# Kernel optimization log

Measured on AMD Instinct MI355X. Metric: run time of the kernel, lower is better.

## Reference

```python
import jax, jax.numpy as jnp
import numpy as np

H = 1024      # hidden_size
V = 50257     # output_size (vocab)
L = 512       # max_length


def setup_inputs() -> dict:
    key = jax.random.key(0)
    ks = jax.random.split(key, 12)
    s = 0.02
    return {
        "x": jax.random.randint(ks[0], (1,), 0, V),
        "encoder_outputs": jax.random.normal(ks[1], (L, H), jnp.float32),
        "hidden": jax.random.normal(ks[2], (1, 1, H), jnp.float32),
        # parameters
        "emb": jax.random.normal(ks[3], (V, H), jnp.float32) * s,
        "attn_W": jax.random.normal(ks[4], (L, 2 * H), jnp.float32) * s,
        "attn_b": jnp.zeros((L,), jnp.float32),
        "comb_W": jax.random.normal(ks[5], (H, 2 * H), jnp.float32) * s,
        "comb_b": jnp.zeros((H,), jnp.float32),
        "W_ih": jax.random.normal(ks[6], (3 * H, H), jnp.float32) * s,
        "W_hh": jax.random.normal(ks[7], (3 * H, H), jnp.float32) * s,
        "b_ih": jnp.zeros((3 * H,), jnp.float32),
        "b_hh": jnp.zeros((3 * H,), jnp.float32),
        "out_W": jax.random.normal(ks[8], (V, H), jnp.float32) * s,
        "out_b": jnp.zeros((V,), jnp.float32),
    }


def reference(x, encoder_outputs, hidden, emb, attn_W, attn_b, comb_W, comb_b,
              W_ih, W_hh, b_ih, b_hh, out_W, out_b):
    # embedded: [1, H]  (dropout_p=0 -> identity)
    embedded = emb[x]
    h0 = hidden[0]  # [1, H]
    # Bahdanau-style attention over encoder positions
    attn_weights = jax.nn.softmax(
        jnp.concatenate([embedded, h0], axis=1) @ attn_W.T + attn_b, axis=1)  # [1, L]
    attn_applied = attn_weights @ encoder_outputs  # [1, H]
    # combine + relu
    out = jnp.concatenate([embedded, attn_applied], axis=1) @ comb_W.T + comb_b
    out = jax.nn.relu(out)  # [1, H] -- GRU input
    # GRU cell (PyTorch gate ordering: r, z, n)
    gx = out @ W_ih.T + b_ih   # [1, 3H]
    gh = h0 @ W_hh.T + b_hh    # [1, 3H]
    gx_r, gx_z, gx_n = jnp.split(gx, 3, axis=1)
    gh_r, gh_z, gh_n = jnp.split(gh, 3, axis=1)
    r = jax.nn.sigmoid(gx_r + gh_r)
    z = jax.nn.sigmoid(gx_z + gh_z)
    n = jnp.tanh(gx_n + r * gh_n)
    h_new = (1.0 - z) * n + z * h0  # [1, H]
    # output projection + log_softmax
    logp = jax.nn.log_softmax(h_new @ out_W.T + out_b, axis=1)  # [1, V]
    return logp, attn_weights
```

## Files before the change

kernel.cpp:

```cpp
#include <hip/hip_runtime.h>
#include <math.h>

#define H 1024
#define V 50257
#define L 512
#define RPB 32
#define NPART ((V + RPB - 1) / RPB)

__device__ inline float wave_reduce_sum(float v) {
    #pragma unroll
    for (int off = 32; off > 0; off >>= 1)
        v += __shfl_down(v, off, 64);
    return v;
}

__device__ inline float wave_reduce_max(float v) {
    #pragma unroll
    for (int off = 32; off > 0; off >>= 1)
        v = fmaxf(v, __shfl_down(v, off, 64));
    return v;
}

__device__ inline float dot4(float4 a, float4 b) {
    return a.x * b.x + a.y * b.y + a.z * b.z + a.w * b.w;
}

__device__ inline float sigmoidf_(float x) { return 1.f / (1.f + expf(-x)); }

__global__ void k1_scores_gh(const int* __restrict__ x,
                             const float* __restrict__ emb,
                             const float* __restrict__ hidden,
                             const float* __restrict__ attn_W,
                             const float* __restrict__ attn_b,
                             const float* __restrict__ W_hh,
                             const float* __restrict__ b_hh,
                             float* __restrict__ scores,
                             float* __restrict__ gh,
                             float* __restrict__ attnap) {
    const int b = blockIdx.x;
    const int t = threadIdx.x;
    const int lid = t & 63, wid = t >> 6;
    const float4* hv = (const float4*)hidden;
    if (b < 128) {
        const int l = b * 4 + wid;
        const int xi = x[0];
        const float4* ev = (const float4*)(emb + (size_t)xi * H);
        const float4* wrow = (const float4*)(attn_W + (size_t)l * (2 * H));
        float acc = 0.f;
        #pragma unroll
        for (int k = 0; k < 4; ++k) {
            int idx = k * 64 + lid;
            acc += dot4(ev[idx], wrow[idx]);
        }
        #pragma unroll
        for (int k = 0; k < 4; ++k) {
            int idx = k * 64 + lid;
            acc += dot4(hv[idx], wrow[256 + idx]);
        }
        acc = wave_reduce_sum(acc);
        if (lid == 0) scores[l] = acc + attn_b[l];
    } else if (b < 896) {
        const int r = (b - 128) * 4 + wid;
        const float4* wrow = (const float4*)(W_hh + (size_t)r * H);
        float acc = 0.f;
        #pragma unroll
        for (int k = 0; k < 4; ++k) {
            int idx = k * 64 + lid;
            acc += dot4(hv[idx], wrow[idx]);
        }
        acc = wave_reduce_sum(acc);
        if (lid == 0) gh[r] = acc + b_hh[r];
    } else {
        ((float4*)attnap)[t] = make_float4(0.f, 0.f, 0.f, 0.f);
    }
}

__global__ void k2_softmax_apply(const float* __restrict__ scores,
                                 const float* __restrict__ enc,
                                 float* __restrict__ attnap,
                                 float* __restrict__ out_attn) {
    const int t = threadIdx.x;
    __shared__ float smx[4], sms[4], sw[512];
    float v0 = scores[t], v1 = scores[t + 256];
    float m = wave_reduce_max(fmaxf(v0, v1));
    if ((t & 63) == 0) smx[t >> 6] = m;
    __syncthreads();
    float M = fmaxf(fmaxf(smx[0], smx[1]), fmaxf(smx[2], smx[3]));
    float e0 = expf(v0 - M), e1 = expf(v1 - M);
    float s = wave_reduce_sum(e0 + e1);
    if ((t & 63) == 0) sms[t >> 6] = s;
    __syncthreads();
    float S = sms[0] + sms[1] + sms[2] + sms[3];
    float w0 = e0 / S, w1 = e1 / S;
    sw[t] = w0;
    sw[t + 256] = w1;
    if (blockIdx.x == 0 && blockIdx.y == 0) {
        out_attn[t] = w0;
        out_attn[t + 256] = w1;
    }
    __syncthreads();
    const int h = blockIdx.x * 256 + t;
    const int l0 = blockIdx.y * 32;
    float acc = 0.f;
    #pragma unroll 8
    for (int i = 0; i < 32; ++i)
        acc += sw[l0 + i] * enc[(size_t)(l0 + i) * H + h];
    atomicAdd(&attnap[h], acc);
}

__global__ void k3_combine(const int* __restrict__ x,
                           const float* __restrict__ emb,
                           const float* __restrict__ attnap,
                           const float* __restrict__ comb_W,
                           const float* __restrict__ comb_b,
                           float* __restrict__ gru_in) {
    const int t = threadIdx.x;
    const int lid = t & 63, wid = t >> 6;
    const int r = blockIdx.x * 4 + wid;
    const int xi = x[0];
    const float4* ev = (const float4*)(emb + (size_t)xi * H);
    const float4* av = (const float4*)attnap;
    const float4* wrow = (const float4*)(comb_W + (size_t)r * (2 * H));
    float acc = 0.f;
    #pragma unroll
    for (int k = 0; k < 4; ++k) {
        int idx = k * 64 + lid;
        acc += dot4(ev[idx], wrow[idx]);
    }
    #pragma unroll
    for (int k = 0; k < 4; ++k) {
        int idx = k * 64 + lid;
        acc += dot4(av[idx], wrow[256 + idx]);
    }
    acc = wave_reduce_sum(acc);
    if (lid == 0) gru_in[r] = fmaxf(acc + comb_b[r], 0.f);
}

__global__ void k4_gx(const float* __restrict__ W_ih,
                      const float* __restrict__ b_ih,
                      const float* __restrict__ gru_in,
                      float* __restrict__ gx) {
    const int t = threadIdx.x;
    const int lid = t & 63, wid = t >> 6;
    const int r = blockIdx.x * 4 + wid;
    const float4* vv = (const float4*)gru_in;
    const float4* wrow = (const float4*)(W_ih + (size_t)r * H);
    float acc = 0.f;
    #pragma unroll
    for (int k = 0; k < 4; ++k) {
        int idx = k * 64 + lid;
        acc += dot4(vv[idx], wrow[idx]);
    }
    acc = wave_reduce_sum(acc);
    if (lid == 0) gx[r] = acc + b_ih[r];
}

__global__ void k5_cell_logits(const float* __restrict__ gx,
                               const float* __restrict__ gh,
                               const float* __restrict__ hidden,
                               const float* __restrict__ out_W,
                               const float* __restrict__ out_b,
                               float* __restrict__ logits,
                               float* __restrict__ partials) {
    const int t = threadIdx.x;
    __shared__ float sh[H];
    __shared__ float sl[RPB];
    {
        float4 xr = ((const float4*)gx)[t];
        float4 xz = ((const float4*)(gx + H))[t];
        float4 xn = ((const float4*)(gx + 2 * H))[t];
        float4 hr = ((const float4*)gh)[t];
        float4 hz = ((const float4*)(gh + H))[t];
        float4 hn = ((const float4*)(gh + 2 * H))[t];
        float4 h0 = ((const float4*)hidden)[t];
        float4 o;
        {
            float r = sigmoidf_(xr.x + hr.x), z = sigmoidf_(xz.x + hz.x);
            float n = tanhf(xn.x + r * hn.x);
            o.x = (1.f - z) * n + z * h0.x;
        }
        {
            float r = sigmoidf_(xr.y + hr.y), z = sigmoidf_(xz.y + hz.y);
            float n = tanhf(xn.y + r * hn.y);
            o.y = (1.f - z) * n + z * h0.y;
        }
        {
            float r = sigmoidf_(xr.z + hr.z), z = sigmoidf_(xz.z + hz.z);
            float n = tanhf(xn.z + r * hn.z);
            o.z = (1.f - z) * n + z * h0.z;
        }
        {
            float r = sigmoidf_(xr.w + hr.w), z = sigmoidf_(xz.w + hz.w);
            float n = tanhf(xn.w + r * hn.w);
            o.w = (1.f - z) * n + z * h0.w;
        }
        ((float4*)sh)[t] = o;
    }
    __syncthreads();
    const int lid = t & 63, wid = t >> 6;
    const float4* hv = (const float4*)sh;
    float4 h0 = hv[lid], h1 = hv[64 + lid], h2 = hv[128 + lid], h3 = hv[192 + lid];
    const int vbase = blockIdx.x * RPB + wid * 8;
    float acc[8];
    #pragma unroll
    for (int rr = 0; rr < 8; ++rr) {
        const int v = vbase + rr;
        if (v < V) {
            const float4* wr = (const float4*)(out_W + (size_t)v * H);
            acc[rr] = dot4(wr[lid], h0) + dot4(wr[64 + lid], h1)
                    + dot4(wr[128 + lid], h2) + dot4(wr[192 + lid], h3);
        } else {
            acc[rr] = 0.f;
        }
    }
    #pragma unroll
    for (int rr = 0; rr < 8; ++rr) {
        const int v = vbase + rr;
        float a = wave_reduce_sum(acc[rr]);
        float val = -INFINITY;
        if (lid == 0) {
            if (v < V) { val = a + out_b[v]; logits[v] = val; }
            sl[wid * 8 + rr] = val;
        }
    }
    __syncthreads();
    if (t == 0) {
        float M = -INFINITY;
        #pragma unroll
        for (int i = 0; i < RPB; ++i) M = fmaxf(M, sl[i]);
        float S = 0.f;
        #pragma unroll
        for (int i = 0; i < RPB; ++i) S += expf(sl[i] - M);
        partials[2 * blockIdx.x] = M;
        partials[2 * blockIdx.x + 1] = S;
    }
}

__global__ void k6_finalize(float* __restrict__ logits,
                            const float* __restrict__ partials) {
    const int t = threadIdx.x;
    __shared__ float sm[8];
    float m = -INFINITY;
    for (int i = t; i < NPART; i += 512) m = fmaxf(m, partials[2 * i]);
    m = wave_reduce_max(m);
    if ((t & 63) == 0) sm[t >> 6] = m;
    __syncthreads();
    float M = sm[0];
    #pragma unroll
    for (int i = 1; i < 8; ++i) M = fmaxf(M, sm[i]);
    __syncthreads();
    float s = 0.f;
    for (int i = t; i < NPART; i += 512) s += partials[2 * i + 1] * expf(partials[2 * i] - M);
    s = wave_reduce_sum(s);
    if ((t & 63) == 0) sm[t >> 6] = s;
    __syncthreads();
    float S = 0.f;
    #pragma unroll
    for (int i = 0; i < 8; ++i) S += sm[i];
    const float red = M + logf(S);
    const int v = blockIdx.x * 512 + t;
    if (v < V) logits[v] -= red;
}

extern "C" void kernel_launch(void* const* d_in, const int* in_sizes, int n_in,
                              void* d_out, int out_size, void* d_ws, size_t ws_size,
                              hipStream_t stream) {
    const int*   x       = (const int*)d_in[0];
    const float* enc     = (const float*)d_in[1];
    const float* hidden  = (const float*)d_in[2];
    const float* emb     = (const float*)d_in[3];
    const float* attn_W  = (const float*)d_in[4];
    const float* attn_b  = (const float*)d_in[5];
    const float* comb_W  = (const float*)d_in[6];
    const float* comb_b  = (const float*)d_in[7];
    const float* W_ih    = (const float*)d_in[8];
    const float* W_hh    = (const float*)d_in[9];
    const float* b_ih    = (const float*)d_in[10];
    const float* b_hh    = (const float*)d_in[11];
    const float* out_W   = (const float*)d_in[12];
    const float* out_b   = (const float*)d_in[13];
    float* out = (float*)d_out;
    float* ws  = (float*)d_ws;

    float* scores   = ws;
    float* attnap   = ws + 512;
    float* gru_in   = ws + 1536;
    float* gx       = ws + 2560;
    float* gh       = ws + 5632;
    float* partials = ws + 8704;

    k1_scores_gh<<<897, 256, 0, stream>>>(x, emb, hidden, attn_W, attn_b,
                                          W_hh, b_hh, scores, gh, attnap);
    k2_softmax_apply<<<dim3(4, 16), 256, 0, stream>>>(scores, enc, attnap, out + V);
    k3_combine<<<256, 256, 0, stream>>>(x, emb, attnap, comb_W, comb_b, gru_in);
    k4_gx<<<768, 256, 0, stream>>>(W_ih, b_ih, gru_in, gx);
    k5_cell_logits<<<NPART, 256, 0, stream>>>(gx, gh, hidden, out_W, out_b, out, partials);
    k6_finalize<<<(V + 511) / 512, 512, 0, stream>>>(out, partials);
}
```

Before: 424.4 us.

## Fuse six decoder kernels into one persistent kernel with grid barriers

Replaces the six-kernel launch sequence with a single persistent kernel of 786 blocks that separates stages with software grid-wide barriers (atomic counter plus generation flag). Logits are held in shared memory, so the final log-softmax normalization writes the output once instead of re-reading and rewriting it from global memory. This is meant to remove per-launch overhead and the extra logits round trip. In exchange it depends on all 786 blocks being co-resident (enforced only by launch bounds), spin-waits with a bounded timeout, and leaves most blocks idle during the small attention stages.

```diff
diff --git a/kernel.cpp b/kernel.cpp
--- a/kernel.cpp
+++ b/kernel.cpp
@@ -6,6 +6,8 @@
 #define L 512
 #define RPB 32
 #define NPART ((V + RPB - 1) / RPB)
+#define GRID 786
+#define TOTW (GRID * 4)
 
 __device__ inline float wave_reduce_sum(float v) {
     #pragma unroll
@@ -27,25 +29,134 @@
 
 __device__ inline float sigmoidf_(float x) { return 1.f / (1.f + expf(-x)); }
 
-__global__ void k1_scores_gh(const int* __restrict__ x,
-                             const float* __restrict__ emb,
-                             const float* __restrict__ hidden,
-                             const float* __restrict__ attn_W,
-                             const float* __restrict__ attn_b,
-                             const float* __restrict__ W_hh,
-                             const float* __restrict__ b_hh,
-                             float* __restrict__ scores,
-                             float* __restrict__ gh,
-                             float* __restrict__ attnap) {
-    const int b = blockIdx.x;
-    const int t = threadIdx.x;
+__device__ inline void gbar(unsigned* cnt, unsigned* gen, unsigned idx) {
+    __syncthreads();
+    if (threadIdx.x == 0) {
+        __threadfence();
+        unsigned old = atomicAdd(cnt, 1u);
+        if (old == GRID * (idx + 1u) - 1u) {
+            atomicExch(gen, idx + 1u);
+        } else {
+            int guard = 0;
+            while (__atomic_load_n(gen, __ATOMIC_ACQUIRE) <= idx &&
+                   ++guard < (1 << 24)) {
+                __builtin_amdgcn_s_sleep(2);
+            }
+        }
+        __threadfence();
+    }
+    __syncthreads();
+}
+
+__global__ __launch_bounds__(256, 4) void mega(
+        const int* __restrict__ x,
+        const float* __restrict__ enc,
+        const float* __restrict__ hidden,
+        const float* __restrict__ emb,
+        const float* __restrict__ attn_W,
+        const float* __restrict__ attn_b,
+        const float* __restrict__ comb_W,
+        const float* __restrict__ comb_b,
+        const float* __restrict__ W_ih,
+        const float* __restrict__ W_hh,
+        const float* __restrict__ b_ih,
+        const float* __restrict__ b_hh,
+        const float* __restrict__ out_W,
+        const float* __restrict__ out_b,
+        float* __restrict__ out,
+        float* __restrict__ ws) {
+    float* scores   = ws;
+    float* attnap   = ws + 512;
+    float* gru_in   = ws + 1536;
+    float* gx       = ws + 2560;
+    float* gh       = ws + 5632;
+    float* partials = ws + 8704;
+    unsigned* cnt   = (unsigned*)(ws + 11904);
+    unsigned* gen   = cnt + 1;
+
+    const int t   = threadIdx.x;
     const int lid = t & 63, wid = t >> 6;
-    const float4* hv = (const float4*)hidden;
-    if (b < 128) {
-        const int l = b * 4 + wid;
+    const int gw  = blockIdx.x * 4 + wid;
+
+    __shared__ float sh[H];
+    __shared__ float sw[512];
+    __shared__ float sl[64];
+    __shared__ float smx[4], sms[4];
+
+    {
+        const float4* hv = (const float4*)hidden;
+        for (int row = gw; row < 3584; row += TOTW) {
+            if (row < 512) {
+                const int xi = x[0];
+                const float4* ev   = (const float4*)(emb + (size_t)xi * H);
+                const float4* wrow = (const float4*)(attn_W + (size_t)row * (2 * H));
+                float acc = 0.f;
+                #pragma unroll
+                for (int k = 0; k < 4; ++k) {
+                    int idx = k * 64 + lid;
+                    acc += dot4(ev[idx], wrow[idx]);
+                }
+                #pragma unroll
+                for (int k = 0; k < 4; ++k) {
+                    int idx = k * 64 + lid;
+                    acc += dot4(hv[idx], wrow[256 + idx]);
+                }
+                acc = wave_reduce_sum(acc);
+                if (lid == 0) scores[row] = acc + attn_b[row];
+            } else {
+                const int r = row - 512;
+                const float4* wrow = (const float4*)(W_hh + (size_t)r * H);
+                float acc = 0.f;
+                #pragma unroll
+                for (int k = 0; k < 4; ++k) {
+                    int idx = k * 64 + lid;
+                    acc += dot4(hv[idx], wrow[idx]);
+                }
+                acc = wave_reduce_sum(acc);
+                if (lid == 0) gh[r] = acc + b_hh[r];
+            }
+        }
+        if (blockIdx.x == GRID - 1)
+            ((float4*)attnap)[t] = make_float4(0.f, 0.f, 0.f, 0.f);
+    }
+    gbar(cnt, gen, 0);
+
+    if (blockIdx.x < 64) {
+        const int bx = blockIdx.x & 3, by = blockIdx.x >> 2;
+        float v0 = scores[t], v1 = scores[t + 256];
+        float m = wave_reduce_max(fmaxf(v0, v1));
+        if (lid == 0) smx[wid] = m;
+        __syncthreads();
+        float M = fmaxf(fmaxf(smx[0], smx[1]), fmaxf(smx[2], smx[3]));
+        float e0 = expf(v0 - M), e1 = expf(v1 - M);
+        float s = wave_reduce_sum(e0 + e1);
+        if (lid == 0) sms[wid] = s;
+        __syncthreads();
+        float S = sms[0] + sms[1] + sms[2] + sms[3];
+        float w0 = e0 / S, w1 = e1 / S;
+        sw[t] = w0;
+        sw[t + 256] = w1;
+        if (blockIdx.x == 0) {
+            out[V + t] = w0;
+            out[V + t + 256] = w1;
+        }
+        __syncthreads();
+        const int h  = bx * 256 + t;
+        const int l0 = by * 32;
+        float acc = 0.f;
+        #pragma unroll 8
+        for (int i = 0; i < 32; ++i)
+            acc += sw[l0 + i] * enc[(size_t)(l0 + i) * H + h];
+        atomicAdd(&attnap[h], acc);
+    }
+    gbar(cnt, gen, 1);
+
+    if (gw < 1024) {
+        const int r = gw;
         const int xi = x[0];
-        const float4* ev = (const float4*)(emb + (size_t)xi * H);
-        const float4* wrow = (const float4*)(attn_W + (size_t)l * (2 * H));
+        const float4* ev   = (const float4*)(emb + (size_t)xi * H);
+        const float4* av   = (const float4*)attnap;
+        const float4* wrow = (const float4*)(comb_W + (size_t)r * (2 * H));
         float acc = 0.f;
         #pragma unroll
         for (int k = 0; k < 4; ++k) {
@@ -55,116 +166,28 @@
         #pragma unroll
         for (int k = 0; k < 4; ++k) {
             int idx = k * 64 + lid;
-            acc += dot4(hv[idx], wrow[256 + idx]);
+            acc += dot4(av[idx], wrow[256 + idx]);
         }
         acc = wave_reduce_sum(acc);
-        if (lid == 0) scores[l] = acc + attn_b[l];
-    } else if (b < 896) {
-        const int r = (b - 128) * 4 + wid;
-        const float4* wrow = (const float4*)(W_hh + (size_t)r * H);
+        if (lid == 0) gru_in[r] = fmaxf(acc + comb_b[r], 0.f);
+    }
+    gbar(cnt, gen, 2);
+
+    if (gw < 3072) {
+        const int r = gw;
+        const float4* vv   = (const float4*)gru_in;
+        const float4* wrow = (const float4*)(W_ih + (size_t)r * H);
         float acc = 0.f;
         #pragma unroll
         for (int k = 0; k < 4; ++k) {
             int idx = k * 64 + lid;
-            acc += dot4(hv[idx], wrow[idx]);
+            acc += dot4(vv[idx], wrow[idx]);
         }
         acc = wave_reduce_sum(acc);
-        if (lid == 0) gh[r] = acc + b_hh[r];
-    } else {
-        ((float4*)attnap)[t] = make_float4(0.f, 0.f, 0.f, 0.f);
-    }
-}
-
-__global__ void k2_softmax_apply(const float* __restrict__ scores,
-                                 const float* __restrict__ enc,
-                                 float* __restrict__ attnap,
-                                 float* __restrict__ out_attn) {
-    const int t = threadIdx.x;
-    __shared__ float smx[4], sms[4], sw[512];
-    float v0 = scores[t], v1 = scores[t + 256];
-    float m = wave_reduce_max(fmaxf(v0, v1));
-    if ((t & 63) == 0) smx[t >> 6] = m;
-    __syncthreads();
-    float M = fmaxf(fmaxf(smx[0], smx[1]), fmaxf(smx[2], smx[3]));
-    float e0 = expf(v0 - M), e1 = expf(v1 - M);
-    float s = wave_reduce_sum(e0 + e1);
-    if ((t & 63) == 0) sms[t >> 6] = s;
-    __syncthreads();
-    float S = sms[0] + sms[1] + sms[2] + sms[3];
-    float w0 = e0 / S, w1 = e1 / S;
-    sw[t] = w0;
-    sw[t + 256] = w1;
-    if (blockIdx.x == 0 && blockIdx.y == 0) {
-        out_attn[t] = w0;
-        out_attn[t + 256] = w1;
-    }
-    __syncthreads();
-    const int h = blockIdx.x * 256 + t;
-    const int l0 = blockIdx.y * 32;
-    float acc = 0.f;
-    #pragma unroll 8
-    for (int i = 0; i < 32; ++i)
-        acc += sw[l0 + i] * enc[(size_t)(l0 + i) * H + h];
-    atomicAdd(&attnap[h], acc);
-}
-
-__global__ void k3_combine(const int* __restrict__ x,
-                           const float* __restrict__ emb,
-                           const float* __restrict__ attnap,
-                           const float* __restrict__ comb_W,
-                           const float* __restrict__ comb_b,
-                           float* __restrict__ gru_in) {
-    const int t = threadIdx.x;
-    const int lid = t & 63, wid = t >> 6;
-    const int r = blockIdx.x * 4 + wid;
-    const int xi = x[0];
-    const float4* ev = (const float4*)(emb + (size_t)xi * H);
-    const float4* av = (const float4*)attnap;
-    const float4* wrow = (const float4*)(comb_W + (size_t)r * (2 * H));
-    float acc = 0.f;
-    #pragma unroll
-    for (int k = 0; k < 4; ++k) {
-        int idx = k * 64 + lid;
-        acc += dot4(ev[idx], wrow[idx]);
-    }
-    #pragma unroll
-    for (int k = 0; k < 4; ++k) {
-        int idx = k * 64 + lid;
-        acc += dot4(av[idx], wrow[256 + idx]);
-    }
-    acc = wave_reduce_sum(acc);
-    if (lid == 0) gru_in[r] = fmaxf(acc + comb_b[r], 0.f);
-}
-
-__global__ void k4_gx(const float* __restrict__ W_ih,
-                      const float* __restrict__ b_ih,
-                      const float* __restrict__ gru_in,
-                      float* __restrict__ gx) {
-    const int t = threadIdx.x;
-    const int lid = t & 63, wid = t >> 6;
-    const int r = blockIdx.x * 4 + wid;
-    const float4* vv = (const float4*)gru_in;
-    const float4* wrow = (const float4*)(W_ih + (size_t)r * H);
-    float acc = 0.f;
-    #pragma unroll
-    for (int k = 0; k < 4; ++k) {
-        int idx = k * 64 + lid;
-        acc += dot4(vv[idx], wrow[idx]);
-    }
-    acc = wave_reduce_sum(acc);
-    if (lid == 0) gx[r] = acc + b_ih[r];
-}
-
-__global__ void k5_cell_logits(const float* __restrict__ gx,
-                               const float* __restrict__ gh,
-                               const float* __restrict__ hidden,
-                               const float* __restrict__ out_W,
-                               const float* __restrict__ out_b,
-                               float* __restrict__ logits,
-                               float* __restrict__ partials) {
-    const int t = threadIdx.x;
-    __shared__ float sh[H];
-    __shared__ float sl[RPB];
+        if (lid == 0) gx[r] = acc + b_ih[r];
+    }
+    gbar(cnt, gen, 3);
+
     {
         float4 xr = ((const float4*)gx)[t];
         float4 xz = ((const float4*)(gx + H))[t];
@@ -197,69 +220,78 @@
         ((float4*)sh)[t] = o;
     }
     __syncthreads();
-    const int lid = t & 63, wid = t >> 6;
-    const float4* hv = (const float4*)sh;
-    float4 h0 = hv[lid], h1 = hv[64 + lid], h2 = hv[128 + lid], h3 = hv[192 + lid];
-    const int vbase = blockIdx.x * RPB + wid * 8;
-    float acc[8];
-    #pragma unroll
-    for (int rr = 0; rr < 8; ++rr) {
-        const int v = vbase + rr;
-        if (v < V) {
-            const float4* wr = (const float4*)(out_W + (size_t)v * H);
-            acc[rr] = dot4(wr[lid], h0) + dot4(wr[64 + lid], h1)
-                    + dot4(wr[128 + lid], h2) + dot4(wr[192 + lid], h3);
-        } else {
-            acc[rr] = 0.f;
-        }
-    }
-    #pragma unroll
-    for (int rr = 0; rr < 8; ++rr) {
-        const int v = vbase + rr;
-        float a = wave_reduce_sum(acc[rr]);
-        float val = -INFINITY;
-        if (lid == 0) {
-            if (v < V) { val = a + out_b[v]; logits[v] = val; }
-            sl[wid * 8 + rr] = val;
+    {
+        const float4* hv4 = (const float4*)sh;
+        float4 hh0 = hv4[lid], hh1 = hv4[64 + lid], hh2 = hv4[128 + lid], hh3 = hv4[192 + lid];
+        #pragma unroll 1
+        for (int ci = 0; ci < 2; ++ci) {
+            const int c = blockIdx.x + ci * GRID;
+            if (c >= NPART) break;
+            const int vbase = c * RPB + wid * 8;
+            float acc[8];
+            #pragma unroll
+            for (int rr = 0; rr < 8; ++rr) {
+                const int v = vbase + rr;
+                if (v < V) {
+                    const float4* wr = (const float4*)(out_W + (size_t)v * H);
+                    acc[rr] = dot4(wr[lid], hh0) + dot4(wr[64 + lid], hh1)
+                            + dot4(wr[128 + lid], hh2) + dot4(wr[192 + lid], hh3);
+                } else {
+                    acc[rr] = 0.f;
+                }
+            }
+            #pragma unroll
+            for (int rr = 0; rr < 8; ++rr) {
+                float a = wave_reduce_sum(acc[rr]);
+                if (lid == 0) {
+                    const int v = vbase + rr;
+                    sl[ci * 32 + wid * 8 + rr] = (v < V) ? (a + out_b[v]) : -INFINITY;
+                }
+            }
         }
     }
     __syncthreads();
     if (t == 0) {
-        float M = -INFINITY;
-        #pragma unroll
-        for (int i = 0; i < RPB; ++i) M = fmaxf(M, sl[i]);
-        float S = 0.f;
-        #pragma unroll
-        for (int i = 0; i < RPB; ++i) S += expf(sl[i] - M);
-        partials[2 * blockIdx.x] = M;
-        partials[2 * blockIdx.x + 1] = S;
-    }
-}
-
-__global__ void k6_finalize(float* __restrict__ logits,
-                            const float* __restrict__ partials) {
-    const int t = threadIdx.x;
-    __shared__ float sm[8];
-    float m = -INFINITY;
-    for (int i = t; i < NPART; i += 512) m = fmaxf(m, partials[2 * i]);
-    m = wave_reduce_max(m);
-    if ((t & 63) == 0) sm[t >> 6] = m;
-    __syncthreads();
-    float M = sm[0];
-    #pragma unroll
-    for (int i = 1; i < 8; ++i) M = fmaxf(M, sm[i]);
-    __syncthreads();
-    float s = 0.f;
-    for (int i = t; i < NPART; i += 512) s += partials[2 * i + 1] * expf(partials[2 * i] - M);
-    s = wave_reduce_sum(s);
-    if ((t & 63) == 0) sm[t >> 6] = s;
-    __syncthreads();
-    float S = 0.f;
-    #pragma unroll
-    for (int i = 0; i < 8; ++i) S += sm[i];
-    const float red = M + logf(S);
-    const int v = blockIdx.x * 512 + t;
-    if (v < V) logits[v] -= red;
+        #pragma unroll 1
+        for (int ci = 0; ci < 2; ++ci) {
+            const int c = blockIdx.x + ci * GRID;
+            if (c >= NPART) break;
+            float M = -INFINITY;
+            #pragma unroll
+            for (int i = 0; i < 32; ++i) M = fmaxf(M, sl[ci * 32 + i]);
+            float S = 0.f;
+            #pragma unroll
+            for (int i = 0; i < 32; ++i) S += expf(sl[ci * 32 + i] - M);
+            partials[2 * c] = M;
+            partials[2 * c + 1] = S;
+        }
+    }
+    gbar(cnt, gen, 4);
+
+    {
+        float m = -INFINITY;
+        for (int i = t; i < NPART; i += 256) m = fmaxf(m, partials[2 * i]);
+        m = wave_reduce_max(m);
+        if (lid == 0) smx[wid] = m;
+        __syncthreads();
+        float M = fmaxf(fmaxf(smx[0], smx[1]), fmaxf(smx[2], smx[3]));
+        float s = 0.f;
+        for (int i = t; i < NPART; i += 256)
+            s += partials[2 * i + 1] * expf(partials[2 * i] - M);
+        s = wave_reduce_sum(s);
+        if (lid == 0) sms[wid] = s;
+        __syncthreads();
+        float S = sms[0] + sms[1] + sms[2] + sms[3];
+        const float red = M + logf(S);
+        if (t < 64) {
+            const int ci = t >> 5;
+            const int c = blockIdx.x + ci * GRID;
+            if (c < NPART) {
+                const int v = c * RPB + (t & 31);
+                if (v < V) out[v] = sl[ci * 32 + (t & 31)] - red;
+            }
+        }
+    }
 }
 
 extern "C" void kernel_launch(void* const* d_in, const int* in_sizes, int n_in,
@@ -282,18 +314,9 @@
     float* out = (float*)d_out;
     float* ws  = (float*)d_ws;
 
-    float* scores   = ws;
-    float* attnap   = ws + 512;
-    float* gru_in   = ws + 1536;
-    float* gx       = ws + 2560;
-    float* gh       = ws + 5632;
-    float* partials = ws + 8704;
-
-    k1_scores_gh<<<897, 256, 0, stream>>>(x, emb, hidden, attn_W, attn_b,
-                                          W_hh, b_hh, scores, gh, attnap);
-    k2_softmax_apply<<<dim3(4, 16), 256, 0, stream>>>(scores, enc, attnap, out + V);
-    k3_combine<<<256, 256, 0, stream>>>(x, emb, attnap, comb_W, comb_b, gru_in);
-    k4_gx<<<768, 256, 0, stream>>>(W_ih, b_ih, gru_in, gx);
-    k5_cell_logits<<<NPART, 256, 0, stream>>>(gx, gh, hidden, out_W, out_b, out, partials);
-    k6_finalize<<<(V + 511) / 512, 512, 0, stream>>>(out, partials);
-}
+    hipMemsetAsync(ws + 11904, 0, 2 * sizeof(unsigned), stream);
+
+    mega<<<GRID, 256, 0, stream>>>(x, enc, hidden, emb, attn_W, attn_b,
+                                   comb_W, comb_b, W_ih, W_hh, b_ih, b_hh,
+                                   out_W, out_b, out, ws);
+}
```

Result: slower. 886.2 us (+108.8%).
